# Optimization experiments

Hardware: AMD Instinct MI355X
Metric: run time of the kernel (lower is better)

The kernel has to match this reference:

```python
import jax, jax.numpy as jnp
import numpy as np

EPS = 1e-12
TOPK = 6

def _l2norm(x):
    # matches torch F.normalize(p=2, eps=1e-12)
    n = jnp.linalg.norm(x, axis=-1, keepdims=True)
    return x / jnp.maximum(n, EPS)

def setup_inputs() -> dict:
    key = jax.random.key(0)
    k1, k2 = jax.random.split(key)
    nC, M, P, d = 5, 512, 196, 384
    support = jax.random.normal(k1, (nC, P, d), dtype=jnp.float32)
    query = jax.random.normal(k2, (M, P, d), dtype=jnp.float32)
    scale_cls = jnp.full((1,), 10.0, dtype=jnp.float32)  # init value in module
    bias = jnp.zeros((1,), dtype=jnp.float32)
    return {"support": support, "query": query, "scale_cls": scale_cls, "bias": bias}

def reference(support, query, scale_cls, bias):
    q = _l2norm(query)      # [M, P, d]
    s = _l2norm(support)    # [nC, P, d]
    # batched cosine similarity between every query patch and support patch
    sim = jnp.einsum('mpd,cqd->mcpq', q, s)   # [M, nC, P, P]
    # max over support patches, then sum of top-6 query-patch matches
    m = sim.max(axis=3)                        # [M, nC, P]
    top6 = jax.lax.top_k(m, TOPK)[0].sum(axis=-1)  # [M, nC]
    cls_scores = top6[None]                    # [1, M, nC] (unsqueeze(0))
    return scale_cls * (cls_scores + bias)
```

## Files before the change

kernel.cpp:

```cpp
#include <hip/hip_runtime.h>
#include <hip/hip_bf16.h>
#include <cstdint>

typedef __attribute__((ext_vector_type(8))) short short8;
typedef __attribute__((ext_vector_type(4))) float floatx4;

#define NC   5
#define PP   196
#define DD   384
#define MM   512
#define ROWS (MM * PP)
#define NRB  1568
#define EPSN 1e-12f

#define TILE_BYTES  49152
#define KSTEP_BYTES 4096

__device__ __forceinline__ unsigned enc_f(float f) {
    unsigned u = __float_as_uint(f);
    return (u & 0x80000000u) ? ~u : (u | 0x80000000u);
}
__device__ __forceinline__ float dec_f(unsigned u) {
    unsigned b = (u & 0x80000000u) ? (u ^ 0x80000000u) : ~u;
    return __uint_as_float(b);
}
#define ENC_NEG_INF 0x007FFFFFu

__global__ __launch_bounds__(256) void k_norm0(const float* __restrict__ sup,
                                               float* __restrict__ sinv) {
    int wid = threadIdx.x >> 6, lane = threadIdx.x & 63;
    int r = blockIdx.x * 4 + wid;
    if (r >= NC * PP) return;
    const float* src = sup + (size_t)r * DD;
    float s = 0.f;
    #pragma unroll
    for (int j = 0; j < 6; ++j) { float v = src[lane + j * 64]; s += v * v; }
    #pragma unroll
    for (int off = 1; off < 64; off <<= 1) s += __shfl_xor(s, off, 64);
    if (lane == 0) sinv[r] = 1.0f / fmaxf(sqrtf(s), EPSN);
}

__global__ __launch_bounds__(256) void k_swz(const float* __restrict__ sup,
                                             const float* __restrict__ sinv,
                                             __hip_bfloat16* __restrict__ snw) {
    int s = blockIdx.x * 256 + threadIdx.x;
    int lane = s & 63;
    int r1 = s >> 6;
    int ct = r1 & 3;
    int r2 = r1 >> 2;
    int kk = r2 % 12;
    int g  = r2 / 12;
    int c = g >> 2, t = g & 3;
    int c16 = lane & 15, quad = lane >> 4;
    int cl = t * 64 + ct * 16 + c16;
    if (cl > PP - 1) cl = PP - 1;
    int srow = c * PP + cl;
    const float* sp = sup + (size_t)srow * DD + kk * 32 + quad * 8;
    float inv = sinv[srow];
    alignas(16) __hip_bfloat16 hb[8];
    #pragma unroll
    for (int e = 0; e < 8; ++e) hb[e] = __float2bfloat16(sp[e] * inv);
    *(uint4*)((char*)snw + (size_t)s * 16) = *(const uint4*)hb;
}

__global__ __launch_bounds__(256, 3) void k_gemm_max(const float* __restrict__ q,
                                                     const __hip_bfloat16* __restrict__ snw,
                                                     float* __restrict__ rowmaxg) {
    __shared__ __hip_bfloat16 As[12 * 4 * 64 * 8];
    __shared__ unsigned rmax[64 * NC];
    __shared__ float rss[64];

    const int tid  = threadIdx.x;
    const int row0 = blockIdx.x * 64;
    const int lane = tid & 63;
    const int wav  = tid >> 6;

    for (int i = tid; i < 64 * NC; i += 256) rmax[i] = ENC_NEG_INF;

    {
        const int arow = tid >> 2;
        const int asub = tid & 3;
        const int rt   = arow >> 4, c16 = arow & 15;
        const float* src = q + (size_t)(row0 + arow) * DD;
        float ss = 0.f;
        #pragma unroll
        for (int i = 0; i < 12; ++i) {
            int ch = asub + i * 4;
            const floatx4* p = (const floatx4*)(src + ch * 8);
            floatx4 x0 = __builtin_nontemporal_load(p);
            floatx4 x1 = __builtin_nontemporal_load(p + 1);
            ss += x0.x*x0.x + x0.y*x0.y + x0.z*x0.z + x0.w*x0.w
                + x1.x*x1.x + x1.y*x1.y + x1.z*x1.z + x1.w*x1.w;
            alignas(16) __hip_bfloat16 hb[8];
            hb[0] = __float2bfloat16(x0.x); hb[1] = __float2bfloat16(x0.y);
            hb[2] = __float2bfloat16(x0.z); hb[3] = __float2bfloat16(x0.w);
            hb[4] = __float2bfloat16(x1.x); hb[5] = __float2bfloat16(x1.y);
            hb[6] = __float2bfloat16(x1.z); hb[7] = __float2bfloat16(x1.w);
            int kk = ch >> 2, quad = ch & 3;
            *(uint4*)&As[(((kk * 4 + rt) * 64) + quad * 16 + c16) * 8] = *(const uint4*)hb;
        }
        ss += __shfl_xor(ss, 1, 64);
        ss += __shfl_xor(ss, 2, 64);
        if (asub == 0) rss[arow] = ss;
    }
    __syncthreads();

    const char* bbase = (const char*)snw + (size_t)wav * TILE_BYTES + (size_t)lane * 16;
    short8 b0[4], b1[4], b2[4], a[4];
    #pragma unroll
    for (int ct = 0; ct < 4; ++ct) b0[ct] = ((const short8*)(bbase + 0 * KSTEP_BYTES))[ct * 64];
    #pragma unroll
    for (int ct = 0; ct < 4; ++ct) b1[ct] = ((const short8*)(bbase + 1 * KSTEP_BYTES))[ct * 64];
    #pragma unroll
    for (int ct = 0; ct < 4; ++ct) b2[ct] = ((const short8*)(bbase + 2 * KSTEP_BYTES))[ct * 64];

    #define LOAD_NEXT(buf, step)                                                     \
        do {                                                                         \
            int nk = kk + 3 + (step);                                                \
            if (nk < 12) {                                                           \
                _Pragma("unroll")                                                    \
                for (int ct = 0; ct < 4; ++ct)                                       \
                    buf[ct] = ((const short8*)(bbase + nk * KSTEP_BYTES))[ct * 64];  \
            } else if (g + 4 < 20) {                                                 \
                _Pragma("unroll")                                                    \
                for (int ct = 0; ct < 4; ++ct)                                       \
                    buf[ct] = ((const short8*)(bbase + 4 * TILE_BYTES +              \
                                               (nk - 12) * KSTEP_BYTES))[ct * 64];   \
            }                                                                        \
        } while (0)

    #define MFMA_STEP(buf, kkoff)                                                    \
        do {                                                                         \
            _Pragma("unroll")                                                        \
            for (int rt = 0; rt < 4; ++rt)                                           \
                a[rt] = *(const short8*)&As[(((kk + (kkoff)) * 4 + rt) * 64 + lane) * 8]; \
            _Pragma("unroll")                                                        \
            for (int rt = 0; rt < 4; ++rt)                                           \
                _Pragma("unroll")                                                    \
                for (int ct = 0; ct < 4; ++ct)                                       \
                    acc[rt][ct] = __builtin_amdgcn_mfma_f32_16x16x32_bf16(           \
                        a[rt], buf[ct], acc[rt][ct], 0, 0, 0);                       \
        } while (0)

    #pragma unroll 1
    for (int g = wav; g < 20; g += 4) {
        floatx4 acc[4][4];
        #pragma unroll
        for (int i = 0; i < 4; ++i)
            #pragma unroll
            for (int j = 0; j < 4; ++j) acc[i][j] = (floatx4){0.f, 0.f, 0.f, 0.f};

        #pragma unroll 1
        for (int kk = 0; kk < 12; kk += 3) {
            MFMA_STEP(b0, 0); LOAD_NEXT(b0, 0);
            MFMA_STEP(b1, 1); LOAD_NEXT(b1, 1);
            MFMA_STEP(b2, 2); LOAD_NEXT(b2, 2);
        }

        const int c = g >> 2;
        const int quad = lane >> 4, c16 = lane & 15;
        #pragma unroll
        for (int rt = 0; rt < 4; ++rt) {
            #pragma unroll
            for (int reg = 0; reg < 4; ++reg) {
                float mx = fmaxf(fmaxf(acc[rt][0][reg], acc[rt][1][reg]),
                                 fmaxf(acc[rt][2][reg], acc[rt][3][reg]));
                #pragma unroll
                for (int off = 1; off < 16; off <<= 1)
                    mx = fmaxf(mx, __shfl_xor(mx, off, 64));
                if (c16 == 0) {
                    int rloc = rt * 16 + quad * 4 + reg;
                    atomicMax(&rmax[rloc * NC + c], enc_f(mx));
                }
            }
        }
        bbase += 4 * TILE_BYTES;
    }

    __syncthreads();
    for (int i = tid; i < 64 * NC; i += 256) {
        int c = i >> 6, row = i & 63;
        float inv = 1.0f / fmaxf(sqrtf(rss[row]), EPSN);
        __builtin_nontemporal_store(dec_f(rmax[row * NC + c]) * inv,
                                    &rowmaxg[(size_t)c * ROWS + row0 + row]);
    }
}

__global__ __launch_bounds__(256) void k_top6(const float* __restrict__ rowmaxg,
                                              const float* __restrict__ scale,
                                              const float* __restrict__ bias,
                                              float* __restrict__ out) {
    int wav = threadIdx.x >> 6, lane = threadIdx.x & 63;
    int pair = blockIdx.x * 4 + wav;
    if (pair >= MM * NC) return;
    int m = pair / NC, c = pair % NC;
    size_t base = (size_t)c * ROWS + (size_t)m * PP;
    float v[4];
    #pragma unroll
    for (int i = 0; i < 4; ++i) {
        int p = lane + i * 64;
        v[i] = (p < PP) ? rowmaxg[base + p] : -INFINITY;
    }
    float sum = 0.f;
    for (int t = 0; t < 6; ++t) {
        float bv = v[0]; int bi = 0;
        #pragma unroll
        for (int i = 1; i < 4; ++i) { if (v[i] > bv) { bv = v[i]; bi = i; } }
        int gid = bi * 64 + lane;
        #pragma unroll
        for (int off = 1; off < 64; off <<= 1) {
            float ov = __shfl_xor(bv, off, 64);
            int og  = __shfl_xor(gid, off, 64);
            if (ov > bv || (ov == bv && og < gid)) { bv = ov; gid = og; }
        }
        sum += bv;
        if ((gid & 63) == lane) v[gid >> 6] = -INFINITY;
    }
    if (lane == 0) out[pair] = scale[0] * (sum + bias[0]);
}

extern "C" void kernel_launch(void* const* d_in, const int* in_sizes, int n_in,
                              void* d_out, int out_size, void* d_ws, size_t ws_size,
                              hipStream_t stream) {
    const float* support = (const float*)d_in[0];
    const float* query   = (const float*)d_in[1];
    const float* scale   = (const float*)d_in[2];
    const float* bias    = (const float*)d_in[3];
    float* out = (float*)d_out;

    char* ws = (char*)d_ws;
    __hip_bfloat16* snw = (__hip_bfloat16*)ws;
    float* sinv         = (float*)(ws + 983040);
    float* rowmaxg      = (float*)(ws + 983040 + 4096);

    hipLaunchKernelGGL(k_norm0,   dim3(245),  dim3(256), 0, stream, support, sinv);
    hipLaunchKernelGGL(k_swz,     dim3(240),  dim3(256), 0, stream, support, sinv, snw);
    hipLaunchKernelGGL(k_gemm_max,dim3(NRB),  dim3(256), 0, stream, query, snw, rowmaxg);
    hipLaunchKernelGGL(k_top6,    dim3(640),  dim3(256), 0, stream, rowmaxg, scale, bias, out);
}
```

Baseline: 323.6 us.

## Switch GEMM-max kernel to 32x32x16 bf16 MFMA with matching operand layouts

Replaces the 16x16x32 MFMA tiling with 32x32x16 MFMAs accumulating into 2x2 floatx16 tiles. To feed them, the support swizzle kernel and the LDS layout of the query tile are both changed. The epilogue row-max reduction is adapted to the 32x32 output layout, using fewer shuffles and more atomics per row. Prefetch of the next B fragments is made branch-free by padding the swizzled support buffer so out-of-range reads stay in bounds. The aim is better operand reuse per instruction and less control flow in the inner loop, at the cost of a larger workspace and more atomic traffic on LDS.

```diff
diff --git a/kernel.cpp b/kernel.cpp
--- a/kernel.cpp
+++ b/kernel.cpp
@@ -4,6 +4,7 @@
 
 typedef __attribute__((ext_vector_type(8))) short short8;
 typedef __attribute__((ext_vector_type(4))) float floatx4;
+typedef __attribute__((ext_vector_type(16))) float floatx16;
 
 #define NC   5
 #define PP   196
@@ -15,6 +16,7 @@
 
 #define TILE_BYTES  49152
 #define KSTEP_BYTES 4096
+#define SNW_ALLOC   (24 * TILE_BYTES)
 
 __device__ __forceinline__ unsigned enc_f(float f) {
     unsigned u = __float_as_uint(f);
@@ -45,17 +47,16 @@
                                              __hip_bfloat16* __restrict__ snw) {
     int s = blockIdx.x * 256 + threadIdx.x;
     int lane = s & 63;
-    int r1 = s >> 6;
-    int ct = r1 & 3;
-    int r2 = r1 >> 2;
-    int kk = r2 % 12;
-    int g  = r2 / 12;
-    int c = g >> 2, t = g & 3;
-    int c16 = lane & 15, quad = lane >> 4;
-    int cl = t * 64 + ct * 16 + c16;
+    int f = (s >> 6) & 3;
+    int t1 = s >> 8;
+    int kk = t1 % 12;
+    int g  = t1 / 12;
+    int kh = f >> 1, ct = f & 1;
+    int l31 = lane & 31, lh = lane >> 5;
+    int cl = (g & 3) * 64 + ct * 32 + l31;
     if (cl > PP - 1) cl = PP - 1;
-    int srow = c * PP + cl;
-    const float* sp = sup + (size_t)srow * DD + kk * 32 + quad * 8;
+    int srow = (g >> 2) * PP + cl;
+    const float* sp = sup + (size_t)srow * DD + kk * 32 + kh * 16 + lh * 8;
     float inv = sinv[srow];
     alignas(16) __hip_bfloat16 hb[8];
     #pragma unroll
@@ -66,7 +67,7 @@
 __global__ __launch_bounds__(256, 3) void k_gemm_max(const float* __restrict__ q,
                                                      const __hip_bfloat16* __restrict__ snw,
                                                      float* __restrict__ rowmaxg) {
-    __shared__ __hip_bfloat16 As[12 * 4 * 64 * 8];
+    __shared__ __hip_bfloat16 As[12 * 2 * 2 * 64 * 8];
     __shared__ unsigned rmax[64 * NC];
     __shared__ float rss[64];
 
@@ -80,7 +81,8 @@
     {
         const int arow = tid >> 2;
         const int asub = tid & 3;
-        const int rt   = arow >> 4, c16 = arow & 15;
+        const int r32  = arow & 31, rt = arow >> 5;
+        const int kh   = asub >> 1, lh = asub & 1;
         const float* src = q + (size_t)(row0 + arow) * DD;
         float ss = 0.f;
         #pragma unroll
@@ -96,8 +98,8 @@
             hb[2] = __float2bfloat16(x0.z); hb[3] = __float2bfloat16(x0.w);
             hb[4] = __float2bfloat16(x1.x); hb[5] = __float2bfloat16(x1.y);
             hb[6] = __float2bfloat16(x1.z); hb[7] = __float2bfloat16(x1.w);
-            int kk = ch >> 2, quad = ch & 3;
-            *(uint4*)&As[(((kk * 4 + rt) * 64) + quad * 16 + c16) * 8] = *(const uint4*)hb;
+            int idx = ((i * 2 + kh) * 2 + rt) * 64 + lh * 32 + r32;
+            *(uint4*)&As[idx * 8] = *(const uint4*)hb;
         }
         ss += __shfl_xor(ss, 1, 64);
         ss += __shfl_xor(ss, 2, 64);
@@ -106,71 +108,70 @@
     __syncthreads();
 
     const char* bbase = (const char*)snw + (size_t)wav * TILE_BYTES + (size_t)lane * 16;
-    short8 b0[4], b1[4], b2[4], a[4];
-    #pragma unroll
-    for (int ct = 0; ct < 4; ++ct) b0[ct] = ((const short8*)(bbase + 0 * KSTEP_BYTES))[ct * 64];
-    #pragma unroll
-    for (int ct = 0; ct < 4; ++ct) b1[ct] = ((const short8*)(bbase + 1 * KSTEP_BYTES))[ct * 64];
-    #pragma unroll
-    for (int ct = 0; ct < 4; ++ct) b2[ct] = ((const short8*)(bbase + 2 * KSTEP_BYTES))[ct * 64];
-
-    #define LOAD_NEXT(buf, step)                                                     \
+    short8 b0[4], b1[4], b2[4];
+    #pragma unroll
+    for (int f = 0; f < 4; ++f) b0[f] = *(const short8*)(bbase + 0 * KSTEP_BYTES + f * 1024);
+    #pragma unroll
+    for (int f = 0; f < 4; ++f) b1[f] = *(const short8*)(bbase + 1 * KSTEP_BYTES + f * 1024);
+    #pragma unroll
+    for (int f = 0; f < 4; ++f) b2[f] = *(const short8*)(bbase + 2 * KSTEP_BYTES + f * 1024);
+
+    #define PREF(buf, nk_)                                                           \
         do {                                                                         \
-            int nk = kk + 3 + (step);                                                \
-            if (nk < 12) {                                                           \
-                _Pragma("unroll")                                                    \
-                for (int ct = 0; ct < 4; ++ct)                                       \
-                    buf[ct] = ((const short8*)(bbase + nk * KSTEP_BYTES))[ct * 64];  \
-            } else if (g + 4 < 20) {                                                 \
-                _Pragma("unroll")                                                    \
-                for (int ct = 0; ct < 4; ++ct)                                       \
-                    buf[ct] = ((const short8*)(bbase + 4 * TILE_BYTES +              \
-                                               (nk - 12) * KSTEP_BYTES))[ct * 64];   \
-            }                                                                        \
+            int nk = (nk_);                                                          \
+            size_t off = (size_t)nk * KSTEP_BYTES + (nk >= 12 ? 3 * TILE_BYTES : 0); \
+            _Pragma("unroll")                                                        \
+            for (int f = 0; f < 4; ++f)                                              \
+                buf[f] = *(const short8*)(bbase + off + f * 1024);                   \
         } while (0)
 
-    #define MFMA_STEP(buf, kkoff)                                                    \
+    #define STEP(buf, kka)                                                           \
         do {                                                                         \
-            _Pragma("unroll")                                                        \
-            for (int rt = 0; rt < 4; ++rt)                                           \
-                a[rt] = *(const short8*)&As[(((kk + (kkoff)) * 4 + rt) * 64 + lane) * 8]; \
-            _Pragma("unroll")                                                        \
-            for (int rt = 0; rt < 4; ++rt)                                           \
-                _Pragma("unroll")                                                    \
-                for (int ct = 0; ct < 4; ++ct)                                       \
-                    acc[rt][ct] = __builtin_amdgcn_mfma_f32_16x16x32_bf16(           \
-                        a[rt], buf[ct], acc[rt][ct], 0, 0, 0);                       \
+            int kx = (kka);                                                          \
+            short8 a00 = *(const short8*)&As[(((kx*2+0)*2+0)*64 + lane) * 8];         \
+            short8 a01 = *(const short8*)&As[(((kx*2+0)*2+1)*64 + lane) * 8];         \
+            short8 a10 = *(const short8*)&As[(((kx*2+1)*2+0)*64 + lane) * 8];         \
+            short8 a11 = *(const short8*)&As[(((kx*2+1)*2+1)*64 + lane) * 8];         \
+            acc[0][0] = __builtin_amdgcn_mfma_f32_32x32x16_bf16(a00, buf[0], acc[0][0], 0, 0, 0); \
+            acc[0][1] = __builtin_amdgcn_mfma_f32_32x32x16_bf16(a00, buf[1], acc[0][1], 0, 0, 0); \
+            acc[1][0] = __builtin_amdgcn_mfma_f32_32x32x16_bf16(a01, buf[0], acc[1][0], 0, 0, 0); \
+            acc[1][1] = __builtin_amdgcn_mfma_f32_32x32x16_bf16(a01, buf[1], acc[1][1], 0, 0, 0); \
+            acc[0][0] = __builtin_amdgcn_mfma_f32_32x32x16_bf16(a10, buf[2], acc[0][0], 0, 0, 0); \
+            acc[0][1] = __builtin_amdgcn_mfma_f32_32x32x16_bf16(a10, buf[3], acc[0][1], 0, 0, 0); \
+            acc[1][0] = __builtin_amdgcn_mfma_f32_32x32x16_bf16(a11, buf[2], acc[1][0], 0, 0, 0); \
+            acc[1][1] = __builtin_amdgcn_mfma_f32_32x32x16_bf16(a11, buf[3], acc[1][1], 0, 0, 0); \
         } while (0)
 
     #pragma unroll 1
     for (int g = wav; g < 20; g += 4) {
-        floatx4 acc[4][4];
-        #pragma unroll
-        for (int i = 0; i < 4; ++i)
+        floatx16 acc[2][2];
+        #pragma unroll
+        for (int i = 0; i < 2; ++i)
             #pragma unroll
-            for (int j = 0; j < 4; ++j) acc[i][j] = (floatx4){0.f, 0.f, 0.f, 0.f};
+            for (int j = 0; j < 2; ++j)
+                #pragma unroll
+                for (int e = 0; e < 16; ++e) acc[i][j][e] = 0.f;
 
         #pragma unroll 1
         for (int kk = 0; kk < 12; kk += 3) {
-            MFMA_STEP(b0, 0); LOAD_NEXT(b0, 0);
-            MFMA_STEP(b1, 1); LOAD_NEXT(b1, 1);
-            MFMA_STEP(b2, 2); LOAD_NEXT(b2, 2);
+            STEP(b0, kk);     PREF(b0, kk + 3);
+            STEP(b1, kk + 1); PREF(b1, kk + 4);
+            STEP(b2, kk + 2); PREF(b2, kk + 5);
         }
 
         const int c = g >> 2;
-        const int quad = lane >> 4, c16 = lane & 15;
-        #pragma unroll
-        for (int rt = 0; rt < 4; ++rt) {
+        const int h = lane >> 5;
+        #pragma unroll
+        for (int rt = 0; rt < 2; ++rt) {
             #pragma unroll
-            for (int reg = 0; reg < 4; ++reg) {
-                float mx = fmaxf(fmaxf(acc[rt][0][reg], acc[rt][1][reg]),
-                                 fmaxf(acc[rt][2][reg], acc[rt][3][reg]));
-                #pragma unroll
-                for (int off = 1; off < 16; off <<= 1)
-                    mx = fmaxf(mx, __shfl_xor(mx, off, 64));
-                if (c16 == 0) {
-                    int rloc = rt * 16 + quad * 4 + reg;
-                    atomicMax(&rmax[rloc * NC + c], enc_f(mx));
+            for (int reg = 0; reg < 16; ++reg) {
+                float m = fmaxf(acc[rt][0][reg], acc[rt][1][reg]);
+                m = fmaxf(m, __shfl_xor(m, 1, 64));
+                m = fmaxf(m, __shfl_xor(m, 2, 64));
+                m = fmaxf(m, __shfl_xor(m, 4, 64));
+                if ((lane & 7) == 0) {
+                    int row = rt * 32 + (reg & 3) + 8 * (reg >> 2) + 4 * h;
+                    atomicMax(&rmax[row * NC + c], enc_f(m));
                 }
             }
         }
@@ -230,8 +231,8 @@
 
     char* ws = (char*)d_ws;
     __hip_bfloat16* snw = (__hip_bfloat16*)ws;
-    float* sinv         = (float*)(ws + 983040);
-    float* rowmaxg      = (float*)(ws + 983040 + 4096);
+    float* sinv         = (float*)(ws + SNW_ALLOC);
+    float* rowmaxg      = (float*)(ws + SNW_ALLOC + 4096);
 
     hipLaunchKernelGGL(k_norm0,   dim3(245),  dim3(256), 0, stream, support, sinv);
     hipLaunchKernelGGL(k_swz,     dim3(240),  dim3(256), 0, stream, support, sinv, snw);
```

Result: slower. 347.4 us (+7.4%).
